# Kernel optimization log

Hardware: AMD Instinct MI355X
Metric: run time of the kernel (lower is better)

## Reference

```python
import jax, jax.numpy as jnp
import numpy as np

B, T, D, H, O = 64, 256, 1024, 1024, 1024


def setup_inputs() -> dict:
    key = jax.random.key(0)
    ks = jax.random.split(key, 20)
    s_w = 1.0 / np.sqrt(H)
    inp = {
        "x": jax.random.normal(ks[0], (B, T, D), jnp.float32),
        "h0": jax.random.normal(ks[1], (B, H), jnp.float32) * 0.1,
        "c0": jax.random.normal(ks[2], (B, H), jnp.float32) * 0.1,
        "W_i": jax.random.normal(ks[3], (D, H), jnp.float32) * s_w,
        "W_f": jax.random.normal(ks[4], (D, H), jnp.float32) * s_w,
        "W_j": jax.random.normal(ks[5], (D, H), jnp.float32) * s_w,
        "W_o": jax.random.normal(ks[6], (D, H), jnp.float32) * s_w,
        "U_i": jax.random.normal(ks[7], (H, H), jnp.float32) * s_w,
        "U_f": jax.random.normal(ks[8], (H, H), jnp.float32) * s_w,
        "U_j": jax.random.normal(ks[9], (H, H), jnp.float32) * s_w,
        "U_o": jax.random.normal(ks[10], (H, H), jnp.float32) * s_w,
        "b_i": jax.random.normal(ks[11], (H,), jnp.float32) * 0.01,
        "b_f": jax.random.normal(ks[12], (H,), jnp.float32) * 0.01,
        "b_j": jax.random.normal(ks[13], (H,), jnp.float32) * 0.01,
        "b_o": jax.random.normal(ks[14], (H,), jnp.float32) * 0.01,
        "W_y": jax.random.normal(ks[15], (H, O), jnp.float32) * s_w,
        "b_y": jax.random.normal(ks[16], (O,), jnp.float32) * 0.01,
    }
    return inp


def reference(x, h0, c0, W_i, W_f, W_j, W_o, U_i, U_f, U_j, U_o,
              b_i, b_f, b_j, b_o, W_y, b_y):
    H_ = h0.shape[-1]
    # Batch the 4 gate input projections into one GEMM over all timesteps.
    W = jnp.concatenate([W_i, W_f, W_j, W_o], axis=1)          # [D, 4H]
    b = jnp.concatenate([b_i, b_f, b_j, b_o])                   # [4H]
    U = jnp.concatenate([U_i, U_f, U_j, U_o], axis=1)           # [H, 4H]
    gx = jnp.einsum('btd,dg->tbg', x, W) + b                    # [T, B, 4H]

    def step(carry, gx_t):
        h, c = carry
        g = gx_t + h @ U                                        # [B, 4H]
        i = jax.nn.sigmoid(g[:, :H_])
        f = jax.nn.sigmoid(g[:, H_:2 * H_])
        j = jnp.tanh(g[:, 2 * H_:3 * H_])
        o = jax.nn.sigmoid(g[:, 3 * H_:])
        c = f * c + i * j
        h = o * jnp.tanh(c)
        return (h, c), h

    (_, _), hs = jax.lax.scan(step, (h0, c0), gx)               # hs: [T, B, H]
    hs = jnp.swapaxes(hs, 0, 1)                                 # [B, T, H]
    y_hat = jnp.einsum('bth,ho->bto', hs, W_y) + b_y            # [B, T, O]
    return y_hat
```

## Files before the change

### kernel.cpp

```cpp
#include <hip/hip_runtime.h>
#include <math.h>

#define Bb 64
#define Tt 256
#define Dd 1024
#define Hh 1024
#define Oo 1024

__device__ __forceinline__ void gbar(unsigned* cnt, unsigned* gen, unsigned nb) {
  __syncthreads();
  if (threadIdx.x == 0) {
    __threadfence();
    unsigned g = __hip_atomic_load(gen, __ATOMIC_RELAXED, __HIP_MEMORY_SCOPE_AGENT);
    if (__hip_atomic_fetch_add(cnt, 1u, __ATOMIC_ACQ_REL, __HIP_MEMORY_SCOPE_AGENT) == nb - 1u) {
      __hip_atomic_store(cnt, 0u, __ATOMIC_RELAXED, __HIP_MEMORY_SCOPE_AGENT);
      __hip_atomic_store(gen, g + 1u, __ATOMIC_RELEASE, __HIP_MEMORY_SCOPE_AGENT);
    } else {
      unsigned spins = 0;
      while (__hip_atomic_load(gen, __ATOMIC_ACQUIRE, __HIP_MEMORY_SCOPE_AGENT) == g) {
        __builtin_amdgcn_s_sleep(8);
        if (++spins > (1u << 18)) break;
      }
    }
  }
  __syncthreads();
}

__device__ __forceinline__ unsigned short f32_to_bf16(float f) {
  unsigned u = __float_as_uint(f);
  u += 0x7FFFu + ((u >> 16) & 1u);
  return (unsigned short)(u >> 16);
}

template <bool PACKED, bool HSBF16>
__global__ __launch_bounds__(256) void lstm_fused(
    const float* __restrict__ x, const float* __restrict__ h0,
    const float* __restrict__ c0,
    const float* __restrict__ U0, const float* __restrict__ U1,
    const float* __restrict__ U2, const float* __restrict__ U3,
    const float* __restrict__ W0, const float* __restrict__ W1,
    const float* __restrict__ W2, const float* __restrict__ W3,
    const float* __restrict__ bi, const float* __restrict__ bf_,
    const float* __restrict__ bj, const float* __restrict__ bo,
    void* __restrict__ hsT, float* ht0, float* ht1,
    float* __restrict__ Uc, float* __restrict__ Wc, unsigned* bar) {
  const int nb = blockIdx.x;
  const int s0 = nb << 2;
  const int tid = threadIdx.x;
  const int lane = tid & 63;
  const int q  = tid >> 6;
  const int ws = lane >> 4;
  const int bb = lane & 15;
  const int b0 = bb << 2;

  __shared__ float G2[16 * 68];

  float* __restrict__ Ub = PACKED ? Uc + (size_t)nb * 16384 : nullptr;
  float* __restrict__ Wb = PACKED ? Wc + (size_t)nb * 16384 : nullptr;

  if (PACKED) {
#pragma unroll
    for (int it = 0; it < 16; ++it) {
      const int qq = it & 3;
      const int k = ((it >> 2) << 8) + tid;
      const float* __restrict__ Uq =
          ((qq == 0) ? U0 : (qq == 1) ? U1 : (qq == 2) ? U2 : U3) + s0;
      const float* __restrict__ Wq =
          ((qq == 0) ? W0 : (qq == 1) ? W1 : (qq == 2) ? W2 : W3) + s0;
      *(float4*)&Ub[k * 16 + qq * 4] = *(const float4*)(Uq + (size_t)k * Hh);
      *(float4*)&Wb[k * 16 + qq * 4] = *(const float4*)(Wq + (size_t)k * Hh);
    }
  }

  const int un = tid >> 6, ub = tid & 63;
  float c = c0[(size_t)ub * Hh + s0 + un];
  ht0[(size_t)(s0 + un) * Bb + ub] = h0[(size_t)ub * Hh + s0 + un];
  float bu[4];
  bu[0] = bi[s0 + un]; bu[1] = bf_[s0 + un];
  bu[2] = bj[s0 + un]; bu[3] = bo[s0 + un];

  gbar(bar, bar + 1, gridDim.x);

  const float* __restrict__ UqD =
      ((q == 0) ? U0 : (q == 1) ? U1 : (q == 2) ? U2 : U3) + s0 + (size_t)ws * Hh;
  const float* __restrict__ WqD =
      ((q == 0) ? W0 : (q == 1) ? W1 : (q == 2) ? W2 : W3) + s0;

  const float* __restrict__ xr0 = x + ((size_t)(b0 + 0) * Tt) * Dd + 4 * ws;
  const float* __restrict__ xr1 = x + ((size_t)(b0 + 1) * Tt) * Dd + 4 * ws;
  const float* __restrict__ xr2 = x + ((size_t)(b0 + 2) * Tt) * Dd + 4 * ws;
  const float* __restrict__ xr3 = x + ((size_t)(b0 + 3) * Tt) * Dd + 4 * ws;

  for (int t = 0; t < Tt; ++t) {
    const float* __restrict__ A = (t & 1) ? ht1 : ht0;
    float* __restrict__ Anext = (t & 1) ? ht0 : ht1;

    float acc[4][4] = {};

    {
      const float* __restrict__ Ap = A + (size_t)ws * Bb + b0;
      const float* __restrict__ Up = PACKED ? (Ub + ws * 16 + q * 4) : UqD;
      const size_t ustep = PACKED ? 64 : 4 * (size_t)Hh;
#pragma unroll 8
      for (int k = 0; k < 256; ++k) {
        float4 av = *(const float4*)Ap;
        float4 uv = *(const float4*)Up;
        Ap += 4 * Bb;
        Up += ustep;
        float aa[4] = {av.x, av.y, av.z, av.w};
        float uu[4] = {uv.x, uv.y, uv.z, uv.w};
#pragma unroll
        for (int j = 0; j < 4; ++j)
#pragma unroll
          for (int i = 0; i < 4; ++i) acc[j][i] += aa[i] * uu[j];
      }
    }

    {
      const size_t xoff = (size_t)t * Dd;
#pragma unroll 4
      for (int j = 0; j < 64; ++j) {
        float a[4][4];
        *(float4*)a[0] = *(const float4*)(xr0 + xoff + 16 * j);
        *(float4*)a[1] = *(const float4*)(xr1 + xoff + 16 * j);
        *(float4*)a[2] = *(const float4*)(xr2 + xoff + 16 * j);
        *(float4*)a[3] = *(const float4*)(xr3 + xoff + 16 * j);
        float w[4][4];
#pragma unroll
        for (int kk = 0; kk < 4; ++kk) {
          if (PACKED)
            *(float4*)w[kk] = *(const float4*)(Wb + (size_t)(ws * 64 + j * 256 + kk * 16) + q * 4);
          else
            *(float4*)w[kk] = *(const float4*)(WqD + (size_t)(4 * (ws + 4 * j) + kk) * Hh);
        }
#pragma unroll
        for (int kk = 0; kk < 4; ++kk)
#pragma unroll
          for (int jc = 0; jc < 4; ++jc)
#pragma unroll
            for (int i = 0; i < 4; ++i) acc[jc][i] += a[i][kk] * w[kk][jc];
      }
    }

#pragma unroll
    for (int j = 0; j < 4; ++j)
#pragma unroll
      for (int i = 0; i < 4; ++i) {
        float v = acc[j][i];
        v += __shfl_xor(v, 16);
        v += __shfl_xor(v, 32);
        acc[j][i] = v;
      }
    if (ws == 0) {
#pragma unroll
      for (int j = 0; j < 4; ++j) {
        float4 v = {acc[j][0], acc[j][1], acc[j][2], acc[j][3]};
        *(float4*)&G2[(q * 4 + j) * 68 + b0] = v;
      }
    }
    __syncthreads();

    float g4[4];
#pragma unroll
    for (int qq = 0; qq < 4; ++qq)
      g4[qq] = G2[(qq * 4 + un) * 68 + ub] + bu[qq];

    float i_ = 1.f / (1.f + __expf(-g4[0]));
    float f_ = 1.f / (1.f + __expf(-g4[1]));
    float j_ = tanhf(g4[2]);
    float o_ = 1.f / (1.f + __expf(-g4[3]));
    c = f_ * c + i_ * j_;
    float h = o_ * tanhf(c);
    Anext[(size_t)(s0 + un) * Bb + ub] = h;
    const size_t hidx = ((size_t)t * Hh + s0 + un) * Bb + ub;
    if (HSBF16)
      ((unsigned short*)hsT)[hidx] = f32_to_bf16(h);
    else
      ((float*)hsT)[hidx] = h;

    gbar(bar, bar + 1, gridDim.x);
  }
}

template <bool HSBF16>
__global__ __launch_bounds__(256) void y_gemm(const void* __restrict__ hsT,
                                              const float* __restrict__ Wy,
                                              const float* __restrict__ by,
                                              float* __restrict__ y) {
  const int ot = blockIdx.x;
  const int t  = blockIdx.y;
  const int o0 = (ot << 6) + ((threadIdx.x >> 4) << 2);
  const int b0 = (threadIdx.x & 15) << 2;

  float bias[4];
  *(float4*)bias = *(const float4*)(by + o0);
  float acc[4][4];
#pragma unroll
  for (int i = 0; i < 4; ++i)
#pragma unroll
    for (int j = 0; j < 4; ++j) acc[i][j] = bias[j];

  const float* __restrict__ Af =
      HSBF16 ? nullptr : (const float*)hsT + (size_t)t * Hh * Bb;
  const unsigned short* __restrict__ Ah =
      HSBF16 ? (const unsigned short*)hsT + (size_t)t * Hh * Bb : nullptr;

  for (int k = 0; k < Hh; ++k) {
    float aa[4];
    if (HSBF16) {
      ushort4 av = *(const ushort4*)(Ah + (size_t)k * Bb + b0);
      aa[0] = __uint_as_float((unsigned)av.x << 16);
      aa[1] = __uint_as_float((unsigned)av.y << 16);
      aa[2] = __uint_as_float((unsigned)av.z << 16);
      aa[3] = __uint_as_float((unsigned)av.w << 16);
    } else {
      float4 av = *(const float4*)(Af + (size_t)k * Bb + b0);
      aa[0] = av.x; aa[1] = av.y; aa[2] = av.z; aa[3] = av.w;
    }
    float4 uv = *(const float4*)(Wy + (size_t)k * Oo + o0);
    float uu[4] = {uv.x, uv.y, uv.z, uv.w};
#pragma unroll
    for (int i = 0; i < 4; ++i)
#pragma unroll
      for (int j = 0; j < 4; ++j) acc[i][j] += aa[i] * uu[j];
  }

#pragma unroll
  for (int i = 0; i < 4; ++i) {
    float4 v = {acc[i][0], acc[i][1], acc[i][2], acc[i][3]};
    *(float4*)(y + ((size_t)(b0 + i) * Tt + t) * Oo + o0) = v;
  }
}

extern "C" void kernel_launch(void* const* d_in, const int* in_sizes, int n_in,
                              void* d_out, int out_size, void* d_ws, size_t ws_size,
                              hipStream_t stream) {
  const float* x  = (const float*)d_in[0];
  const float* h0 = (const float*)d_in[1];
  const float* c0 = (const float*)d_in[2];
  const float* W0 = (const float*)d_in[3];
  const float* W1 = (const float*)d_in[4];
  const float* W2 = (const float*)d_in[5];
  const float* W3 = (const float*)d_in[6];
  const float* U0 = (const float*)d_in[7];
  const float* U1 = (const float*)d_in[8];
  const float* U2 = (const float*)d_in[9];
  const float* U3 = (const float*)d_in[10];
  const float* bi = (const float*)d_in[11];
  const float* bf_ = (const float*)d_in[12];
  const float* bj = (const float*)d_in[13];
  const float* bo = (const float*)d_in[14];
  const float* Wy = (const float*)d_in[15];
  const float* by = (const float*)d_in[16];
  float* y = (float*)d_out;

  const size_t pk_elems = (size_t)256 * 16384;
  const size_t hs_elems = (size_t)Tt * Hh * Bb;
  const size_t ht_elems = (size_t)Hh * Bb;
  const size_t needA = (2 * pk_elems + hs_elems + 2 * ht_elems) * 4 + 64;
  const size_t needB = 2 * pk_elems * 4 + hs_elems * 2 + 2 * ht_elems * 4 + 64;
  const int tier = (ws_size >= needA) ? 0 : (ws_size >= needB) ? 1 : 2;

  char* base = (char*)d_ws;
  float *Uc = nullptr, *Wc = nullptr;
  void* hsT;
  float *ht0, *ht1;
  unsigned* bar;
  if (tier <= 1) {
    Uc = (float*)base;
    Wc = Uc + pk_elems;
    hsT = (void*)(Wc + pk_elems);
  } else {
    hsT = (void*)base;
  }
  const size_t hs_bytes = (tier == 0) ? hs_elems * 4 : hs_elems * 2;
  ht0 = (float*)((char*)hsT + hs_bytes);
  ht1 = ht0 + ht_elems;
  bar = (unsigned*)(ht1 + ht_elems);

  hipMemsetAsync(bar, 0, 64, stream);

  if (tier == 0)
    lstm_fused<true, false><<<256, 256, 0, stream>>>(
        x, h0, c0, U0, U1, U2, U3, W0, W1, W2, W3, bi, bf_, bj, bo, hsT, ht0,
        ht1, Uc, Wc, bar);
  else if (tier == 1)
    lstm_fused<true, true><<<256, 256, 0, stream>>>(
        x, h0, c0, U0, U1, U2, U3, W0, W1, W2, W3, bi, bf_, bj, bo, hsT, ht0,
        ht1, Uc, Wc, bar);
  else
    lstm_fused<false, true><<<256, 256, 0, stream>>>(
        x, h0, c0, U0, U1, U2, U3, W0, W1, W2, W3, bi, bf_, bj, bo, hsT, ht0,
        ht1, Uc, Wc, bar);

  dim3 gy(16, 256);
  if (tier == 0)
    y_gemm<false><<<gy, 256, 0, stream>>>(hsT, Wy, by, y);
  else
    y_gemm<true><<<gy, 256, 0, stream>>>(hsT, Wy, by, y);
}
```

Before: 25.51 ms.

## Use two-level grid barrier, 512-thread split-K blocks, and bf16 packed recurrent weights

Replaces the flat single-counter grid barrier with a two-level tree (16 leaf counters plus a root) and shortens the spin sleep, to cut atomic contention in the 256 per-timestep barriers. Doubles the block size to 512 threads and splits the K dimension across two waves per gate, adding a cross-wave reduction in shared memory. The packed recurrent weights U are stored in bf16, halving their traffic, and the hidden-state history is always kept in bf16. This lowers the precision of the recurrent matmul, and the rounding error can compound across timesteps.

```diff
diff --git a/kernel.cpp b/kernel.cpp
--- a/kernel.cpp
+++ b/kernel.cpp
@@ -7,19 +7,28 @@
 #define Hh 1024
 #define Oo 1024
 
-__device__ __forceinline__ void gbar(unsigned* cnt, unsigned* gen, unsigned nb) {
+__device__ __forceinline__ void gbar(unsigned* bar, int leaf) {
   __syncthreads();
   if (threadIdx.x == 0) {
     __threadfence();
+    unsigned* leafc = bar + leaf * 16;
+    unsigned* rootc = bar + 256;
+    unsigned* gen   = bar + 272;
     unsigned g = __hip_atomic_load(gen, __ATOMIC_RELAXED, __HIP_MEMORY_SCOPE_AGENT);
-    if (__hip_atomic_fetch_add(cnt, 1u, __ATOMIC_ACQ_REL, __HIP_MEMORY_SCOPE_AGENT) == nb - 1u) {
-      __hip_atomic_store(cnt, 0u, __ATOMIC_RELAXED, __HIP_MEMORY_SCOPE_AGENT);
-      __hip_atomic_store(gen, g + 1u, __ATOMIC_RELEASE, __HIP_MEMORY_SCOPE_AGENT);
-    } else {
+    bool done = false;
+    if (__hip_atomic_fetch_add(leafc, 1u, __ATOMIC_ACQ_REL, __HIP_MEMORY_SCOPE_AGENT) == 15u) {
+      __hip_atomic_store(leafc, 0u, __ATOMIC_RELAXED, __HIP_MEMORY_SCOPE_AGENT);
+      if (__hip_atomic_fetch_add(rootc, 1u, __ATOMIC_ACQ_REL, __HIP_MEMORY_SCOPE_AGENT) == 15u) {
+        __hip_atomic_store(rootc, 0u, __ATOMIC_RELAXED, __HIP_MEMORY_SCOPE_AGENT);
+        __hip_atomic_store(gen, g + 1u, __ATOMIC_RELEASE, __HIP_MEMORY_SCOPE_AGENT);
+        done = true;
+      }
+    }
+    if (!done) {
       unsigned spins = 0;
       while (__hip_atomic_load(gen, __ATOMIC_ACQUIRE, __HIP_MEMORY_SCOPE_AGENT) == g) {
-        __builtin_amdgcn_s_sleep(8);
-        if (++spins > (1u << 18)) break;
+        __builtin_amdgcn_s_sleep(2);
+        if (++spins > (1u << 20)) break;
       }
     }
   }
@@ -31,9 +40,11 @@
   u += 0x7FFFu + ((u >> 16) & 1u);
   return (unsigned short)(u >> 16);
 }
-
-template <bool PACKED, bool HSBF16>
-__global__ __launch_bounds__(256) void lstm_fused(
+__device__ __forceinline__ float blo(unsigned u) { return __uint_as_float(u << 16); }
+__device__ __forceinline__ float bhi(unsigned u) { return __uint_as_float(u & 0xFFFF0000u); }
+
+template <bool PACKED>
+__global__ __launch_bounds__(512) void lstm_fused(
     const float* __restrict__ x, const float* __restrict__ h0,
     const float* __restrict__ c0,
     const float* __restrict__ U0, const float* __restrict__ U1,
@@ -42,54 +53,63 @@
     const float* __restrict__ W2, const float* __restrict__ W3,
     const float* __restrict__ bi, const float* __restrict__ bf_,
     const float* __restrict__ bj, const float* __restrict__ bo,
-    void* __restrict__ hsT, float* ht0, float* ht1,
-    float* __restrict__ Uc, float* __restrict__ Wc, unsigned* bar) {
+    unsigned short* __restrict__ hsT, float* ht0, float* ht1,
+    unsigned short* __restrict__ Uc16, float* __restrict__ Wc,
+    unsigned* bar) {
   const int nb = blockIdx.x;
   const int s0 = nb << 2;
   const int tid = threadIdx.x;
-  const int lane = tid & 63;
-  const int q  = tid >> 6;
-  const int ws = lane >> 4;
-  const int bb = lane & 15;
+  const int w = tid >> 6, lane = tid & 63;
+  const int q = w >> 1, kh = w & 1;
+  const int ws = lane >> 4, bb = lane & 15;
   const int b0 = bb << 2;
-
-  __shared__ float G2[16 * 68];
-
-  float* __restrict__ Ub = PACKED ? Uc + (size_t)nb * 16384 : nullptr;
+  const int kbase = kh * 512 + ws * 128;
+
+  __shared__ float G2[8 * 4 * 68];
+
+  unsigned short* __restrict__ Ub16 =
+      PACKED ? Uc16 + (size_t)nb * 16384 : nullptr;
   float* __restrict__ Wb = PACKED ? Wc + (size_t)nb * 16384 : nullptr;
 
   if (PACKED) {
 #pragma unroll
-    for (int it = 0; it < 16; ++it) {
-      const int qq = it & 3;
-      const int k = ((it >> 2) << 8) + tid;
+    for (int it = 0; it < 8; ++it) {
+      const int qq = it >> 1;
+      const int k = ((it & 1) << 9) + tid;
       const float* __restrict__ Uq =
           ((qq == 0) ? U0 : (qq == 1) ? U1 : (qq == 2) ? U2 : U3) + s0;
       const float* __restrict__ Wq =
           ((qq == 0) ? W0 : (qq == 1) ? W1 : (qq == 2) ? W2 : W3) + s0;
-      *(float4*)&Ub[k * 16 + qq * 4] = *(const float4*)(Uq + (size_t)k * Hh);
-      *(float4*)&Wb[k * 16 + qq * 4] = *(const float4*)(Wq + (size_t)k * Hh);
+      float4 uv = *(const float4*)(Uq + (size_t)k * Hh);
+      float4 wv = *(const float4*)(Wq + (size_t)k * Hh);
+      *(float4*)&Wb[(size_t)k * 16 + qq * 4] = wv;
+      ushort4 us = {f32_to_bf16(uv.x), f32_to_bf16(uv.y), f32_to_bf16(uv.z),
+                    f32_to_bf16(uv.w)};
+      *(ushort4*)&Ub16[((size_t)qq * 1024 + k) * 4] = us;
     }
   }
 
   const int un = tid >> 6, ub = tid & 63;
-  float c = c0[(size_t)ub * Hh + s0 + un];
-  ht0[(size_t)(s0 + un) * Bb + ub] = h0[(size_t)ub * Hh + s0 + un];
-  float bu[4];
-  bu[0] = bi[s0 + un]; bu[1] = bf_[s0 + un];
-  bu[2] = bj[s0 + un]; bu[3] = bo[s0 + un];
-
-  gbar(bar, bar + 1, gridDim.x);
+  float c = 0.f, bu[4] = {0.f, 0.f, 0.f, 0.f};
+  if (tid < 256) {
+    c = c0[(size_t)ub * Hh + s0 + un];
+    ht0[(size_t)(s0 + un) * Bb + ub] = h0[(size_t)ub * Hh + s0 + un];
+    bu[0] = bi[s0 + un]; bu[1] = bf_[s0 + un];
+    bu[2] = bj[s0 + un]; bu[3] = bo[s0 + un];
+  }
+
+  const int leaf = nb >> 4;
+  gbar(bar, leaf);
 
   const float* __restrict__ UqD =
-      ((q == 0) ? U0 : (q == 1) ? U1 : (q == 2) ? U2 : U3) + s0 + (size_t)ws * Hh;
+      ((q == 0) ? U0 : (q == 1) ? U1 : (q == 2) ? U2 : U3) + s0;
   const float* __restrict__ WqD =
       ((q == 0) ? W0 : (q == 1) ? W1 : (q == 2) ? W2 : W3) + s0;
 
-  const float* __restrict__ xr0 = x + ((size_t)(b0 + 0) * Tt) * Dd + 4 * ws;
-  const float* __restrict__ xr1 = x + ((size_t)(b0 + 1) * Tt) * Dd + 4 * ws;
-  const float* __restrict__ xr2 = x + ((size_t)(b0 + 2) * Tt) * Dd + 4 * ws;
-  const float* __restrict__ xr3 = x + ((size_t)(b0 + 3) * Tt) * Dd + 4 * ws;
+  const float* __restrict__ xr0 = x + ((size_t)(b0 + 0) * Tt) * Dd + kbase;
+  const float* __restrict__ xr1 = x + ((size_t)(b0 + 1) * Tt) * Dd + kbase;
+  const float* __restrict__ xr2 = x + ((size_t)(b0 + 2) * Tt) * Dd + kbase;
+  const float* __restrict__ xr3 = x + ((size_t)(b0 + 3) * Tt) * Dd + kbase;
 
   for (int t = 0; t < Tt; ++t) {
     const float* __restrict__ A = (t & 1) ? ht1 : ht0;
@@ -98,47 +118,67 @@
     float acc[4][4] = {};
 
     {
-      const float* __restrict__ Ap = A + (size_t)ws * Bb + b0;
-      const float* __restrict__ Up = PACKED ? (Ub + ws * 16 + q * 4) : UqD;
-      const size_t ustep = PACKED ? 64 : 4 * (size_t)Hh;
+      const size_t xoff = (size_t)t * Dd;
+#pragma unroll 4
+      for (int jl = 0; jl < 32; ++jl) {
+        float a[4][4];
+        *(float4*)a[0] = *(const float4*)(xr0 + xoff + 4 * jl);
+        *(float4*)a[1] = *(const float4*)(xr1 + xoff + 4 * jl);
+        *(float4*)a[2] = *(const float4*)(xr2 + xoff + 4 * jl);
+        *(float4*)a[3] = *(const float4*)(xr3 + xoff + 4 * jl);
+        float wv[4][4];
+#pragma unroll
+        for (int kk = 0; kk < 4; ++kk) {
+          const int krow = kbase + 4 * jl + kk;
+          if (PACKED)
+            *(float4*)wv[kk] = *(const float4*)(Wb + (size_t)krow * 16 + q * 4);
+          else
+            *(float4*)wv[kk] = *(const float4*)(WqD + (size_t)krow * Hh);
+        }
+#pragma unroll
+        for (int kk = 0; kk < 4; ++kk)
+#pragma unroll
+          for (int jc = 0; jc < 4; ++jc)
+#pragma unroll
+            for (int i = 0; i < 4; ++i) acc[jc][i] += a[i][kk] * wv[kk][jc];
+      }
+    }
+
+    if (PACKED) {
+      const float* __restrict__ Ap = A + (size_t)kbase * Bb + b0;
+      const uint4* __restrict__ Upq =
+          (const uint4*)(Ub16 + ((size_t)q * 1024 + kbase) * 4);
 #pragma unroll 8
-      for (int k = 0; k < 256; ++k) {
+      for (int k2 = 0; k2 < 64; ++k2) {
+        float4 a0 = *(const float4*)Ap;
+        float4 a1 = *(const float4*)(Ap + Bb);
+        Ap += 2 * Bb;
+        uint4 up = Upq[k2];
+        float u0[4] = {blo(up.x), bhi(up.x), blo(up.y), bhi(up.y)};
+        float u1[4] = {blo(up.z), bhi(up.z), blo(up.w), bhi(up.w)};
+        float aa0[4] = {a0.x, a0.y, a0.z, a0.w};
+        float aa1[4] = {a1.x, a1.y, a1.z, a1.w};
+#pragma unroll
+        for (int j = 0; j < 4; ++j)
+#pragma unroll
+          for (int i = 0; i < 4; ++i)
+            acc[j][i] += aa0[i] * u0[j] + aa1[i] * u1[j];
+      }
+    } else {
+      const float* __restrict__ Ap = A + (size_t)kbase * Bb + b0;
+      const float* __restrict__ Up = UqD + (size_t)kbase * Hh;
+#pragma unroll 8
+      for (int k = 0; k < 128; ++k) {
         float4 av = *(const float4*)Ap;
         float4 uv = *(const float4*)Up;
-        Ap += 4 * Bb;
-        Up += ustep;
+        Ap += Bb;
+        Up += Hh;
         float aa[4] = {av.x, av.y, av.z, av.w};
         float uu[4] = {uv.x, uv.y, uv.z, uv.w};
 #pragma unroll
         for (int j = 0; j < 4; ++j)
 #pragma unroll
           for (int i = 0; i < 4; ++i) acc[j][i] += aa[i] * uu[j];
-      }
-    }
-
-    {
-      const size_t xoff = (size_t)t * Dd;
-#pragma unroll 4
-      for (int j = 0; j < 64; ++j) {
-        float a[4][4];
-        *(float4*)a[0] = *(const float4*)(xr0 + xoff + 16 * j);
-        *(float4*)a[1] = *(const float4*)(xr1 + xoff + 16 * j);
-        *(float4*)a[2] = *(const float4*)(xr2 + xoff + 16 * j);
-        *(float4*)a[3] = *(const float4*)(xr3 + xoff + 16 * j);
-        float w[4][4];
-#pragma unroll
-        for (int kk = 0; kk < 4; ++kk) {
-          if (PACKED)
-            *(float4*)w[kk] = *(const float4*)(Wb + (size_t)(ws * 64 + j * 256 + kk * 16) + q * 4);
-          else
-            *(float4*)w[kk] = *(const float4*)(WqD + (size_t)(4 * (ws + 4 * j) + kk) * Hh);
-        }
-#pragma unroll
-        for (int kk = 0; kk < 4; ++kk)
-#pragma unroll
-          for (int jc = 0; jc < 4; ++jc)
-#pragma unroll
-            for (int i = 0; i < 4; ++i) acc[jc][i] += a[i][kk] * w[kk][jc];
       }
     }
 
@@ -155,38 +195,35 @@
 #pragma unroll
       for (int j = 0; j < 4; ++j) {
         float4 v = {acc[j][0], acc[j][1], acc[j][2], acc[j][3]};
-        *(float4*)&G2[(q * 4 + j) * 68 + b0] = v;
+        *(float4*)&G2[((size_t)w * 4 + j) * 68 + b0] = v;
       }
     }
     __syncthreads();
 
-    float g4[4];
-#pragma unroll
-    for (int qq = 0; qq < 4; ++qq)
-      g4[qq] = G2[(qq * 4 + un) * 68 + ub] + bu[qq];
-
-    float i_ = 1.f / (1.f + __expf(-g4[0]));
-    float f_ = 1.f / (1.f + __expf(-g4[1]));
-    float j_ = tanhf(g4[2]);
-    float o_ = 1.f / (1.f + __expf(-g4[3]));
-    c = f_ * c + i_ * j_;
-    float h = o_ * tanhf(c);
-    Anext[(size_t)(s0 + un) * Bb + ub] = h;
-    const size_t hidx = ((size_t)t * Hh + s0 + un) * Bb + ub;
-    if (HSBF16)
-      ((unsigned short*)hsT)[hidx] = f32_to_bf16(h);
-    else
-      ((float*)hsT)[hidx] = h;
-
-    gbar(bar, bar + 1, gridDim.x);
-  }
-}
-
-template <bool HSBF16>
-__global__ __launch_bounds__(256) void y_gemm(const void* __restrict__ hsT,
-                                              const float* __restrict__ Wy,
-                                              const float* __restrict__ by,
-                                              float* __restrict__ y) {
+    if (tid < 256) {
+      float g4[4];
+#pragma unroll
+      for (int qq = 0; qq < 4; ++qq)
+        g4[qq] = G2[((size_t)(qq * 2 + 0) * 4 + un) * 68 + ub] +
+                 G2[((size_t)(qq * 2 + 1) * 4 + un) * 68 + ub] + bu[qq];
+
+      float i_ = 1.f / (1.f + __expf(-g4[0]));
+      float f_ = 1.f / (1.f + __expf(-g4[1]));
+      float j_ = tanhf(g4[2]);
+      float o_ = 1.f / (1.f + __expf(-g4[3]));
+      c = f_ * c + i_ * j_;
+      float h = o_ * tanhf(c);
+      Anext[(size_t)(s0 + un) * Bb + ub] = h;
+      hsT[((size_t)t * Hh + s0 + un) * Bb + ub] = f32_to_bf16(h);
+    }
+
+    gbar(bar, leaf);
+  }
+}
+
+__global__ __launch_bounds__(256) void y_gemm(
+    const unsigned short* __restrict__ hsT, const float* __restrict__ Wy,
+    const float* __restrict__ by, float* __restrict__ y) {
   const int ot = blockIdx.x;
   const int t  = blockIdx.y;
   const int o0 = (ot << 6) + ((threadIdx.x >> 4) << 2);
@@ -200,23 +237,13 @@
 #pragma unroll
     for (int j = 0; j < 4; ++j) acc[i][j] = bias[j];
 
-  const float* __restrict__ Af =
-      HSBF16 ? nullptr : (const float*)hsT + (size_t)t * Hh * Bb;
-  const unsigned short* __restrict__ Ah =
-      HSBF16 ? (const unsigned short*)hsT + (size_t)t * Hh * Bb : nullptr;
-
+  const unsigned short* __restrict__ Ah = hsT + (size_t)t * Hh * Bb;
   for (int k = 0; k < Hh; ++k) {
-    float aa[4];
-    if (HSBF16) {
-      ushort4 av = *(const ushort4*)(Ah + (size_t)k * Bb + b0);
-      aa[0] = __uint_as_float((unsigned)av.x << 16);
-      aa[1] = __uint_as_float((unsigned)av.y << 16);
-      aa[2] = __uint_as_float((unsigned)av.z << 16);
-      aa[3] = __uint_as_float((unsigned)av.w << 16);
-    } else {
-      float4 av = *(const float4*)(Af + (size_t)k * Bb + b0);
-      aa[0] = av.x; aa[1] = av.y; aa[2] = av.z; aa[3] = av.w;
-    }
+    ushort4 av = *(const ushort4*)(Ah + (size_t)k * Bb + b0);
+    float aa[4] = {__uint_as_float((unsigned)av.x << 16),
+                   __uint_as_float((unsigned)av.y << 16),
+                   __uint_as_float((unsigned)av.z << 16),
+                   __uint_as_float((unsigned)av.w << 16)};
     float4 uv = *(const float4*)(Wy + (size_t)k * Oo + o0);
     float uu[4] = {uv.x, uv.y, uv.z, uv.w};
 #pragma unroll
@@ -254,48 +281,40 @@
   const float* by = (const float*)d_in[16];
   float* y = (float*)d_out;
 
-  const size_t pk_elems = (size_t)256 * 16384;
+  const size_t uc_elems = (size_t)256 * 16384;
+  const size_t wc_elems = (size_t)256 * 16384;
   const size_t hs_elems = (size_t)Tt * Hh * Bb;
   const size_t ht_elems = (size_t)Hh * Bb;
-  const size_t needA = (2 * pk_elems + hs_elems + 2 * ht_elems) * 4 + 64;
-  const size_t needB = 2 * pk_elems * 4 + hs_elems * 2 + 2 * ht_elems * 4 + 64;
-  const int tier = (ws_size >= needA) ? 0 : (ws_size >= needB) ? 1 : 2;
+  const size_t need = uc_elems * 2 + wc_elems * 4 + hs_elems * 2 +
+                      2 * ht_elems * 4 + 4096;
+  const bool packed = (ws_size >= need);
 
   char* base = (char*)d_ws;
-  float *Uc = nullptr, *Wc = nullptr;
-  void* hsT;
-  float *ht0, *ht1;
-  unsigned* bar;
-  if (tier <= 1) {
-    Uc = (float*)base;
-    Wc = Uc + pk_elems;
-    hsT = (void*)(Wc + pk_elems);
+  unsigned short* Uc16 = nullptr;
+  float* Wc = nullptr;
+  unsigned short* hsT;
+  if (packed) {
+    Uc16 = (unsigned short*)base;
+    Wc = (float*)(base + uc_elems * 2);
+    hsT = (unsigned short*)(base + uc_elems * 2 + wc_elems * 4);
   } else {
-    hsT = (void*)base;
-  }
-  const size_t hs_bytes = (tier == 0) ? hs_elems * 4 : hs_elems * 2;
-  ht0 = (float*)((char*)hsT + hs_bytes);
-  ht1 = ht0 + ht_elems;
-  bar = (unsigned*)(ht1 + ht_elems);
-
-  hipMemsetAsync(bar, 0, 64, stream);
-
-  if (tier == 0)
-    lstm_fused<true, false><<<256, 256, 0, stream>>>(
+    hsT = (unsigned short*)base;
+  }
+  float* ht0 = (float*)((char*)hsT + hs_elems * 2);
+  float* ht1 = ht0 + ht_elems;
+  unsigned* bar = (unsigned*)(ht1 + ht_elems);
+
+  hipMemsetAsync(bar, 0, 2048, stream);
+
+  if (packed)
+    lstm_fused<true><<<256, 512, 0, stream>>>(
         x, h0, c0, U0, U1, U2, U3, W0, W1, W2, W3, bi, bf_, bj, bo, hsT, ht0,
-        ht1, Uc, Wc, bar);
-  else if (tier == 1)
-    lstm_fused<true, true><<<256, 256, 0, stream>>>(
+        ht1, Uc16, Wc, bar);
+  else
+    lstm_fused<false><<<256, 512, 0, stream>>>(
         x, h0, c0, U0, U1, U2, U3, W0, W1, W2, W3, bi, bf_, bj, bo, hsT, ht0,
-        ht1, Uc, Wc, bar);
-  else
-    lstm_fused<false, true><<<256, 256, 0, stream>>>(
-        x, h0, c0, U0, U1, U2, U3, W0, W1, W2, W3, bi, bf_, bj, bo, hsT, ht0,
-        ht1, Uc, Wc, bar);
+        ht1, Uc16, Wc, bar);
 
   dim3 gy(16, 256);
-  if (tier == 0)
-    y_gemm<false><<<gy, 256, 0, stream>>>(hsT, Wy, by, y);
-  else
-    y_gemm<true><<<gy, 256, 0, stream>>>(hsT, Wy, by, y);
-}
+  y_gemm<<<gy, 256, 0, stream>>>(hsT, Wy, by, y);
+}
```

Result: faster. 24.93 ms (-2.3%).
